# Optimization experiments

Hardware: AMD Instinct MI355X
Metric: run time of the kernel (lower is better)

The kernel has to match this reference:

```python
import jax, jax.numpy as jnp
import numpy as np

N, E, F, H, C, K = 50000, 1600000, 128, 64, 40, 4


def setup_inputs() -> dict:
    key = jax.random.key(0)
    ks = jax.random.split(key, 4)
    x = jax.random.normal(ks[0], (N, F), dtype=jnp.float32)
    edge_index = jax.random.randint(ks[1], (2, E), 0, N, dtype=jnp.int32)
    edge_weight = jnp.ones((E,), dtype=jnp.float32)
    # lin of ChebConv: Linear(K*in, out); kaiming for layer1, xavier-ish for layer2
    W1 = jax.random.normal(ks[2], (K * F, H), dtype=jnp.float32) * (2.0 / (K * F)) ** 0.5
    b1 = jnp.zeros((H,), jnp.float32)
    W2 = jax.random.normal(ks[3], (K * H, C), dtype=jnp.float32) * (2.0 / (K * H + C)) ** 0.5
    b2 = jnp.zeros((C,), jnp.float32)
    return {"x": x, "edge_index": edge_index, "edge_weight": edge_weight,
            "W1": W1, "b1": b1, "W2": W2, "b2": b2}


def _cheb_norm(edge_index, edge_weight, num_nodes):
    """Edge weights of L_hat = 2*L/lambda_max - I with sym norm, lambda_max=2.
    L = I - D^{-1/2} A D^{-1/2}; so L_hat off-diag = -d_i^{-1/2} w d_j^{-1/2},
    diag = (1 if deg>0 else 0) - 1."""
    src, dst = edge_index[0], edge_index[1]
    deg = jax.ops.segment_sum(edge_weight, src, num_segments=num_nodes)
    dis = jnp.where(deg > 0, jax.lax.rsqrt(jnp.maximum(deg, 1e-12)), 0.0)
    w_norm = -dis[src] * edge_weight * dis[dst]   # [E] off-diagonal of L_hat
    diag = jnp.where(deg > 0, 0.0, -1.0)          # [N] diagonal of L_hat
    return src, dst, w_norm, diag


def _cheb_conv(x, src, dst, w_norm, diag, W, b, num_nodes):
    def prop(h):  # L_hat @ h via gather-multiply-scatter
        msg = w_norm[:, None] * h[src]                                  # [E, F]
        return diag[:, None] * h + jax.ops.segment_sum(msg, dst, num_segments=num_nodes)

    Tx_prev2 = x
    Tx_prev1 = prop(x)
    Txs = [Tx_prev2, Tx_prev1]
    for _ in range(2, K):
        Tx = 2.0 * prop(Tx_prev1) - Tx_prev2
        Txs.append(Tx)
        Tx_prev2, Tx_prev1 = Tx_prev1, Tx
    Z = jnp.concatenate(Txs, axis=1)              # [N, K*F]
    return Z @ W + b


def reference(x, edge_index, edge_weight, W1, b1, W2, b2):
    num_nodes = x.shape[0]
    src, dst, w_norm, diag = _cheb_norm(edge_index, edge_weight, num_nodes)
    # dropout layers are identity at inference
    h = _cheb_conv(x, src, dst, w_norm, diag, W1, b1, num_nodes)
    h = jax.nn.relu(h)
    out = _cheb_conv(h, src, dst, w_norm, diag, W2, b2, num_nodes)
    return out
```

## Files before the change

kernel.cpp:

```cpp
#include <hip/hip_runtime.h>

#define NN 50000
#define EE 1600000
#define FF 128
#define HH 64
#define CC 40

#define NCH 64
#define CHE (EE / NCH)
#define NSL 4
#define SLN (NN / NSL)

#define PA 250
#define EPP (EE / PA)
#define SB 250
#define SLNB 200
#define BCAP 64

static __device__ __forceinline__ float bf2f(unsigned short u) {
    union { unsigned int i; float f; } c; c.i = ((unsigned int)u) << 16; return c.f;
}
static __device__ __forceinline__ unsigned short f2bf(float x) {
    union { float f; unsigned int i; } c; c.f = x;
    unsigned int r = c.i + 0x7FFFu + ((c.i >> 16) & 1u);
    return (unsigned short)(r >> 16);
}

__global__ __launch_bounds__(1024) void deg_hist_kernel(
    const int* __restrict__ src, const float* __restrict__ w,
    float* __restrict__ pdeg) {
    __shared__ float ldeg[SLN];
    int s = blockIdx.x % NSL;
    int c = blockIdx.x / NSL;
    int base = s * SLN;
    for (int i = threadIdx.x; i < SLN; i += 1024) ldeg[i] = 0.f;
    __syncthreads();
    int e0 = c * CHE;
    for (int e = e0 + threadIdx.x; e < e0 + CHE; e += 1024) {
        int se = src[e];
        unsigned us = (unsigned)(se - base);
        if (us < SLN) atomicAdd(&ldeg[us], w[e]);
    }
    __syncthreads();
    for (int i = threadIdx.x; i < SLN; i += 1024)
        pdeg[(size_t)c * NN + base + i] = ldeg[i];
}

__global__ void reduce_kernel(const float* __restrict__ pdeg,
                              float* __restrict__ dis, float* __restrict__ diag) {
    int n = blockIdx.x * blockDim.x + threadIdx.x;
    if (n >= NN) return;
    float dsum = 0.f;
    for (int c = 0; c < NCH; ++c) dsum += pdeg[(size_t)c * NN + n];
    dis[n]  = (dsum > 0.f) ? rsqrtf(fmaxf(dsum, 1e-12f)) : 0.f;
    diag[n] = (dsum > 0.f) ? 0.f : -1.f;
}

__global__ __launch_bounds__(256) void bucketA_kernel(
    const int* __restrict__ src, const int* __restrict__ dst,
    const float* __restrict__ w, const float* __restrict__ dis,
    uint2* __restrict__ buckets, int* __restrict__ counts) {
    __shared__ int lcnt[SB];
    int p = blockIdx.x;
    for (int i = threadIdx.x; i < SB; i += 256) lcnt[i] = 0;
    __syncthreads();
    int e0 = p * EPP;
    for (int e = e0 + threadIdx.x; e < e0 + EPP; e += 256) {
        int de = dst[e], se = src[e];
        int sl = de / SLNB;
        int dl = de - sl * SLNB;
        float wn = -dis[se] * w[e] * dis[de];
        unsigned lo = (unsigned)se | ((unsigned)f2bf(wn) << 16);
        int idx = atomicAdd(&lcnt[sl], 1);
        buckets[((size_t)p * SB + sl) * BCAP + idx] = make_uint2(lo, (unsigned)dl);
    }
    __syncthreads();
    for (int i = threadIdx.x; i < SB; i += 256) counts[p * SB + i] = lcnt[i];
}

__global__ void scanS_kernel(const int* __restrict__ counts, int* __restrict__ sbase) {
    __shared__ int sh[256];
    int t = threadIdx.x;
    int total = 0;
    if (t < SB)
        for (int p = 0; p < PA; ++p) total += counts[p * SB + t];
    sh[t] = total;
    __syncthreads();
    for (int off = 1; off < 256; off <<= 1) {
        int x = (t >= off) ? sh[t - off] : 0;
        __syncthreads();
        sh[t] += x;
        __syncthreads();
    }
    if (t < SB) sbase[t] = sh[t] - total;
    if (t == SB - 1) sbase[SB] = sh[t];
}

__global__ __launch_bounds__(256) void bucketB_kernel(
    const uint2* __restrict__ buckets, const int* __restrict__ counts,
    const int* __restrict__ sbase,
    int* __restrict__ row_start, unsigned int* __restrict__ csr) {
    __shared__ int lcounts[PA];
    __shared__ int lhist[SLNB];
    __shared__ int sh[256];
    int s = blockIdx.x;
    int t = threadIdx.x;
    if (t < PA) lcounts[t] = counts[t * SB + s];
    for (int i = t; i < SLNB; i += 256) lhist[i] = 0;
    __syncthreads();
    int g = t >> 4, l16 = t & 15;
    for (int p = g; p < PA; p += 16) {
        int c = lcounts[p];
        const uint2* b = buckets + ((size_t)p * SB + s) * BCAP;
        for (int i = l16; i < c; i += 16)
            atomicAdd(&lhist[b[i].y], 1);
    }
    __syncthreads();
    int v = (t < SLNB) ? lhist[t] : 0;
    sh[t] = v;
    __syncthreads();
    for (int off = 1; off < 256; off <<= 1) {
        int x = (t >= off) ? sh[t - off] : 0;
        __syncthreads();
        sh[t] += x;
        __syncthreads();
    }
    int base = sbase[s];
    if (t < SLNB) {
        int excl = sh[t] - v;
        row_start[s * SLNB + t] = base + excl;
        lhist[t] = base + excl;
    }
    if (s == SB - 1 && t == 0) row_start[NN] = sbase[SB];
    __syncthreads();
    for (int p = g; p < PA; p += 16) {
        int c = lcounts[p];
        const uint2* b = buckets + ((size_t)p * SB + s) * BCAP;
        for (int i = l16; i < c; i += 16) {
            uint2 en = b[i];
            int pos = atomicAdd(&lhist[en.y], 1);
            csr[pos] = en.x;
        }
    }
}

template <int FACT, typename OUT_T>
__global__ __launch_bounds__(256) void prop2_kernel(
    const unsigned short* __restrict__ a, float alphaL,
    const unsigned short* __restrict__ p1, float beta1,
    const unsigned short* __restrict__ p2, float beta2,
    const float* __restrict__ bias, int doRelu, int FOUT, int outStride,
    const float* __restrict__ diag, const int* __restrict__ rs,
    const unsigned int* __restrict__ csr, OUT_T* __restrict__ out) {
    int lane = threadIdx.x & 63;
    int wave = threadIdx.x >> 6;
    int n = blockIdx.x * 4 + wave;
    int f = lane;
    float acc = 0.f;
    if (f < FACT) {
        acc = diag[n] * bf2f(a[(size_t)n * 64 + f]);
        int j0 = rs[n], j1 = rs[n + 1];
        int j = j0;
        for (; j + 8 <= j1; j += 8) {
            unsigned cw[8];
            #pragma unroll
            for (int u = 0; u < 8; ++u) cw[u] = csr[j + u];
            float v[8];
            #pragma unroll
            for (int u = 0; u < 8; ++u)
                v[u] = bf2f(a[(size_t)(cw[u] & 0xFFFFu) * 64 + f]);
            #pragma unroll
            for (int u = 0; u < 8; ++u)
                acc = fmaf(bf2f((unsigned short)(cw[u] >> 16)), v[u], acc);
        }
        for (; j < j1; ++j) {
            unsigned cw = csr[j];
            acc = fmaf(bf2f((unsigned short)(cw >> 16)),
                       bf2f(a[(size_t)(cw & 0xFFFFu) * 64 + f]), acc);
        }
    }
    if (f < FOUT) {
        float r = alphaL * acc + beta1 * bf2f(p1[(size_t)n * 64 + f]);
        if (beta2 != 0.f) r = fmaf(beta2, bf2f(p2[(size_t)n * 64 + f]), r);
        if (bias) r += bias[f];
        if (doRelu) r = fmaxf(r, 0.f);
        OUT_T o;
        if constexpr (sizeof(OUT_T) == 2) o = f2bf(r); else o = r;
        out[(size_t)n * outStride + f] = o;
    }
}

__global__ __launch_bounds__(256) void gemm1_kernel(
    const float* __restrict__ x, const float* __restrict__ W,
    unsigned short* __restrict__ Yb) {
    __shared__ float As[64][36];
    __shared__ float Bs[32][64];
    int t = threadIdx.x;
    int m0 = blockIdx.x * 64;
    int ct = blockIdx.y;
    int tr = t / 16, tc = t % 16;
    int kq = t % 8,  ms = t / 8;
    int jb = t % 16, fb = t / 16;
    float acc[4][4] = {};
    for (int kb = 0; kb < 4; ++kb) {
        __syncthreads();
        #pragma unroll
        for (int p = 0; p < 2; ++p) {
            int m = ms + 32 * p;
            int row = m0 + m;
            float4 vv = make_float4(0.f, 0.f, 0.f, 0.f);
            if (row < NN) vv = *(const float4*)(x + (size_t)row * FF + kb * 32 + kq * 4);
            *(float4*)&As[m][kq * 4] = vv;
        }
        const float* Wb = W + ((size_t)ct * 128 + kb * 32) * HH;
        #pragma unroll
        for (int p = 0; p < 2; ++p) {
            int fi = fb + 16 * p;
            float4 vv = *(const float4*)(Wb + fi * HH + jb * 4);
            *(float4*)&Bs[fi][jb * 4] = vv;
        }
        __syncthreads();
        #pragma unroll 8
        for (int k = 0; k < 32; ++k) {
            float a0 = As[tr * 4 + 0][k], a1 = As[tr * 4 + 1][k];
            float a2 = As[tr * 4 + 2][k], a3 = As[tr * 4 + 3][k];
            float4 b = *(float4*)&Bs[k][tc * 4];
            acc[0][0] = fmaf(a0, b.x, acc[0][0]); acc[0][1] = fmaf(a0, b.y, acc[0][1]);
            acc[0][2] = fmaf(a0, b.z, acc[0][2]); acc[0][3] = fmaf(a0, b.w, acc[0][3]);
            acc[1][0] = fmaf(a1, b.x, acc[1][0]); acc[1][1] = fmaf(a1, b.y, acc[1][1]);
            acc[1][2] = fmaf(a1, b.z, acc[1][2]); acc[1][3] = fmaf(a1, b.w, acc[1][3]);
            acc[2][0] = fmaf(a2, b.x, acc[2][0]); acc[2][1] = fmaf(a2, b.y, acc[2][1]);
            acc[2][2] = fmaf(a2, b.z, acc[2][2]); acc[2][3] = fmaf(a2, b.w, acc[2][3]);
            acc[3][0] = fmaf(a3, b.x, acc[3][0]); acc[3][1] = fmaf(a3, b.y, acc[3][1]);
            acc[3][2] = fmaf(a3, b.z, acc[3][2]); acc[3][3] = fmaf(a3, b.w, acc[3][3]);
        }
    }
    unsigned short* slab = Yb + (size_t)ct * NN * 64;
    #pragma unroll
    for (int r = 0; r < 4; ++r) {
        int n = m0 + tr * 4 + r;
        if (n < NN) {
            ushort4 u4;
            u4.x = f2bf(acc[r][0]); u4.y = f2bf(acc[r][1]);
            u4.z = f2bf(acc[r][2]); u4.w = f2bf(acc[r][3]);
            *(ushort4*)(slab + (size_t)n * 64 + tc * 4) = u4;
        }
    }
}

__global__ __launch_bounds__(256) void gemm2_kernel(
    const float* __restrict__ h, const float* __restrict__ W,
    unsigned short* __restrict__ Zb) {
    __shared__ float As[128][36];
    __shared__ float Bs[32][40];
    int t = threadIdx.x;
    int m0 = blockIdx.x * 128;
    int kt = blockIdx.y;
    int tr = t / 8, tc = t % 8;
    int kq = t % 8, ms = t / 8;
    float acc[4][5] = {};
    for (int kb = 0; kb < 2; ++kb) {
        __syncthreads();
        #pragma unroll
        for (int p = 0; p < 4; ++p) {
            int m = ms + 32 * p;
            int row = m0 + m;
            float4 vv = make_float4(0.f, 0.f, 0.f, 0.f);
            if (row < NN) vv = *(const float4*)(h + (size_t)row * HH + kb * 32 + kq * 4);
            *(float4*)&As[m][kq * 4] = vv;
        }
        const float* Wb = W + ((size_t)kt * 64 + kb * 32) * CC;
        for (int i = t; i < 32 * CC; i += 256) ((float*)Bs)[i] = Wb[i];
        __syncthreads();
        #pragma unroll 4
        for (int k = 0; k < 32; ++k) {
            float a0 = As[tr * 4 + 0][k], a1 = As[tr * 4 + 1][k];
            float a2 = As[tr * 4 + 2][k], a3 = As[tr * 4 + 3][k];
            #pragma unroll
            for (int c = 0; c < 5; ++c) {
                float b = Bs[k][tc * 5 + c];
                acc[0][c] = fmaf(a0, b, acc[0][c]);
                acc[1][c] = fmaf(a1, b, acc[1][c]);
                acc[2][c] = fmaf(a2, b, acc[2][c]);
                acc[3][c] = fmaf(a3, b, acc[3][c]);
            }
        }
    }
    unsigned short* slab = Zb + (size_t)kt * NN * 64;
    #pragma unroll
    for (int r = 0; r < 4; ++r) {
        int n = m0 + tr * 4 + r;
        if (n < NN) {
            unsigned short* brow = slab + (size_t)n * 64;
            #pragma unroll
            for (int c = 0; c < 5; ++c) brow[tc * 5 + c] = f2bf(acc[r][c]);
            if (tc < 6) {
                #pragma unroll
                for (int c = 0; c < 4; ++c) brow[40 + tc * 4 + c] = 0;
            }
        }
    }
}

extern "C" void kernel_launch(void* const* d_in, const int* in_sizes, int n_in,
                              void* d_out, int out_size, void* d_ws, size_t ws_size,
                              hipStream_t stream) {
    const float* x    = (const float*)d_in[0];
    const int*   eidx = (const int*)d_in[1];
    const float* ew   = (const float*)d_in[2];
    const float* W1   = (const float*)d_in[3];
    const float* b1   = (const float*)d_in[4];
    const float* W2   = (const float*)d_in[5];
    const float* b2   = (const float*)d_in[6];
    float* out = (float*)d_out;

    const int* src = eidx;
    const int* dst = eidx + EE;

    float* p = (float*)d_ws;
    unsigned int* csr = (unsigned int*)p;  p += (size_t)EE;
    float* dis  = p;                  p += ((NN + 63) / 64) * 64;
    float* diag = p;                  p += ((NN + 63) / 64) * 64;
    unsigned short* Yb = (unsigned short*)p;  p += (size_t)NN * 128;
    unsigned short* u  = (unsigned short*)p;  p += (size_t)NN * 32;
    unsigned short* v  = (unsigned short*)p;  p += (size_t)NN * 32;
    float* h    = p;                  p += (size_t)NN * 64;
    float* scratch = p;               p += (size_t)PA * SB * BCAP * 2;
    int* row_start = (int*)p;
    int* counts    = row_start + NN + 1;
    int* sbase     = counts + PA * SB;

    float* pdeg    = scratch;
    uint2* buckets = (uint2*)scratch;
    unsigned short* y0b = Yb;
    unsigned short* y1b = Yb + (size_t)1 * NN * 64;
    unsigned short* y2b = Yb + (size_t)2 * NN * 64;
    unsigned short* y3b = Yb + (size_t)3 * NN * 64;
    unsigned short* Zb = Yb;
    unsigned short* z0 = Zb;
    unsigned short* z1 = Zb + (size_t)1 * NN * 64;
    unsigned short* z2 = Zb + (size_t)2 * NN * 64;
    unsigned short* z3 = Zb + (size_t)3 * NN * 64;
    unsigned short* u2 = u;
    unsigned short* v2 = v;

    const int B = 256;
    deg_hist_kernel<<<NCH * NSL, 1024, 0, stream>>>(src, ew, pdeg);
    reduce_kernel<<<(NN + B - 1) / B, B, 0, stream>>>(pdeg, dis, diag);
    bucketA_kernel<<<PA, 256, 0, stream>>>(src, dst, ew, dis, buckets, counts);
    scanS_kernel<<<1, 256, 0, stream>>>(counts, sbase);
    bucketB_kernel<<<SB, 256, 0, stream>>>(buckets, counts, sbase, row_start, csr);

    int pgrid = NN / 4;

    gemm1_kernel<<<dim3((NN + 63) / 64, 4), 256, 0, stream>>>(x, W1, Yb);
    prop2_kernel<64, unsigned short><<<pgrid, 256, 0, stream>>>(
        y3b, 4.f, y2b, 2.f, nullptr, 0.f,
        nullptr, 0, 64, 64, diag, row_start, csr, u);
    prop2_kernel<64, unsigned short><<<pgrid, 256, 0, stream>>>(
        u, 1.f, y1b, 1.f, y3b, -3.f,
        nullptr, 0, 64, 64, diag, row_start, csr, v);
    prop2_kernel<64, float><<<pgrid, 256, 0, stream>>>(
        v, 1.f, y0b, 1.f, y2b, -1.f,
        b1, 1, 64, 64, diag, row_start, csr, h);

    gemm2_kernel<<<dim3((NN + 127) / 128, 4), 256, 0, stream>>>(h, W2, Zb);
    prop2_kernel<48, unsigned short><<<pgrid, 256, 0, stream>>>(
        z3, 4.f, z2, 2.f, nullptr, 0.f,
        nullptr, 0, 48, 64, diag, row_start, csr, u2);
    prop2_kernel<48, unsigned short><<<pgrid, 256, 0, stream>>>(
        u2, 1.f, z1, 1.f, z3, -3.f,
        nullptr, 0, 48, 64, diag, row_start, csr, v2);
    prop2_kernel<48, float><<<pgrid, 256, 0, stream>>>(
        v2, 1.f, z0, 1.f, z2, -1.f,
        b2, 0, 40, 40, diag, row_start, csr, out);
}
```

Measured before the change: 534.3 us.

## Replace FP32 SIMT GEMMs with split-bf16 MFMA GEMMs

Replaces the two shared-memory FP32 FMA GEMM kernels with one templated MFMA kernel that uses bf16 16x16x32 matrix instructions. It keeps near-FP32 accuracy by splitting each operand into hi and lo bf16 parts and issuing three MFMAs per tile. A small kernel pre-transposes and splits W1 and W2 into the scratch buffer, and it pads W2 to 64 output columns with zeros. The aim is to move the dense projection work onto the matrix cores, at the cost of extra conversion instructions, one extra launch, and uncoalesced 2-byte output stores.

New measurement: 520.2 us. 2.6% less time.

```diff
diff --git a/kernel.cpp b/kernel.cpp
--- a/kernel.cpp
+++ b/kernel.cpp
@@ -25,6 +25,10 @@
     unsigned int r = c.i + 0x7FFFu + ((c.i >> 16) & 1u);
     return (unsigned short)(r >> 16);
 }
+
+typedef __attribute__((ext_vector_type(8))) short bf16x8;
+typedef __attribute__((ext_vector_type(4))) float f32x4;
+union BF8 { bf16x8 v; unsigned short u[8]; };
 
 __global__ __launch_bounds__(1024) void deg_hist_kernel(
     const int* __restrict__ src, const float* __restrict__ w,
@@ -190,116 +194,99 @@
     }
 }
 
-__global__ __launch_bounds__(256) void gemm1_kernel(
-    const float* __restrict__ x, const float* __restrict__ W,
-    unsigned short* __restrict__ Yb) {
-    __shared__ float As[64][36];
-    __shared__ float Bs[32][64];
-    int t = threadIdx.x;
-    int m0 = blockIdx.x * 64;
-    int ct = blockIdx.y;
-    int tr = t / 16, tc = t % 16;
-    int kq = t % 8,  ms = t / 8;
-    int jb = t % 16, fb = t / 16;
-    float acc[4][4] = {};
-    for (int kb = 0; kb < 4; ++kb) {
-        __syncthreads();
-        #pragma unroll
-        for (int p = 0; p < 2; ++p) {
-            int m = ms + 32 * p;
-            int row = m0 + m;
-            float4 vv = make_float4(0.f, 0.f, 0.f, 0.f);
-            if (row < NN) vv = *(const float4*)(x + (size_t)row * FF + kb * 32 + kq * 4);
-            *(float4*)&As[m][kq * 4] = vv;
-        }
-        const float* Wb = W + ((size_t)ct * 128 + kb * 32) * HH;
-        #pragma unroll
-        for (int p = 0; p < 2; ++p) {
-            int fi = fb + 16 * p;
-            float4 vv = *(const float4*)(Wb + fi * HH + jb * 4);
-            *(float4*)&Bs[fi][jb * 4] = vv;
-        }
-        __syncthreads();
-        #pragma unroll 8
-        for (int k = 0; k < 32; ++k) {
-            float a0 = As[tr * 4 + 0][k], a1 = As[tr * 4 + 1][k];
-            float a2 = As[tr * 4 + 2][k], a3 = As[tr * 4 + 3][k];
-            float4 b = *(float4*)&Bs[k][tc * 4];
-            acc[0][0] = fmaf(a0, b.x, acc[0][0]); acc[0][1] = fmaf(a0, b.y, acc[0][1]);
-            acc[0][2] = fmaf(a0, b.z, acc[0][2]); acc[0][3] = fmaf(a0, b.w, acc[0][3]);
-            acc[1][0] = fmaf(a1, b.x, acc[1][0]); acc[1][1] = fmaf(a1, b.y, acc[1][1]);
-            acc[1][2] = fmaf(a1, b.z, acc[1][2]); acc[1][3] = fmaf(a1, b.w, acc[1][3]);
-            acc[2][0] = fmaf(a2, b.x, acc[2][0]); acc[2][1] = fmaf(a2, b.y, acc[2][1]);
-            acc[2][2] = fmaf(a2, b.z, acc[2][2]); acc[2][3] = fmaf(a2, b.w, acc[2][3]);
-            acc[3][0] = fmaf(a3, b.x, acc[3][0]); acc[3][1] = fmaf(a3, b.y, acc[3][1]);
-            acc[3][2] = fmaf(a3, b.z, acc[3][2]); acc[3][3] = fmaf(a3, b.w, acc[3][3]);
-        }
-    }
+__global__ __launch_bounds__(256) void convw_kernel(
+    const float* __restrict__ W1, const float* __restrict__ W2,
+    unsigned short* __restrict__ W1t_hi, unsigned short* __restrict__ W1t_lo,
+    unsigned short* __restrict__ W2t_hi, unsigned short* __restrict__ W2t_lo) {
+    int tid = blockIdx.x * 256 + threadIdx.x;
+    if (tid < 512 * 64) {
+        int row = tid >> 7, kk = tid & 127;
+        int ct = row >> 6, j = row & 63;
+        float v = W1[((size_t)(ct * 128 + kk)) * 64 + j];
+        unsigned short h = f2bf(v);
+        W1t_hi[tid] = h;
+        W1t_lo[tid] = f2bf(v - bf2f(h));
+    } else {
+        int t2 = tid - 512 * 64;
+        if (t2 >= 4 * 64 * 64) return;
+        int row = t2 >> 6, kk = t2 & 63;
+        int kt = row >> 6, j = row & 63;
+        float v = (j < CC) ? W2[((size_t)(kt * 64 + kk)) * CC + j] : 0.f;
+        unsigned short h = f2bf(v);
+        W2t_hi[t2] = h;
+        W2t_lo[t2] = f2bf(v - bf2f(h));
+    }
+}
+
+template <int KF>
+__global__ __launch_bounds__(256) void gemm_mfma_kernel(
+    const float* __restrict__ A, const unsigned short* __restrict__ Wt_hi,
+    const unsigned short* __restrict__ Wt_lo, unsigned short* __restrict__ Yb) {
+    constexpr int KK = KF * 32;
+    int lane = threadIdx.x & 63;
+    int ct   = threadIdx.x >> 6;
+    int l15  = lane & 15;
+    int lg   = lane >> 4;
+    int m0   = blockIdx.x * 32;
+
+    f32x4 acc[2][4];
+    #pragma unroll
+    for (int i = 0; i < 2; ++i)
+        #pragma unroll
+        for (int j = 0; j < 4; ++j)
+            acc[i][j] = (f32x4){0.f, 0.f, 0.f, 0.f};
+
+    #pragma unroll
+    for (int kf = 0; kf < KF; ++kf) {
+        int k0 = kf * 32 + lg * 8;
+        BF8 bh[4], bl[4];
+        #pragma unroll
+        for (int nf = 0; nf < 4; ++nf) {
+            size_t addr = (size_t)(ct * 64 + nf * 16 + l15) * KK + k0;
+            bh[nf].v = *reinterpret_cast<const bf16x8*>(Wt_hi + addr);
+            bl[nf].v = *reinterpret_cast<const bf16x8*>(Wt_lo + addr);
+        }
+        BF8 ah[2], al[2];
+        #pragma unroll
+        for (int ms = 0; ms < 2; ++ms) {
+            int n = m0 + ms * 16 + l15;
+            if (n >= NN) n = NN - 1;
+            const float* ap = A + (size_t)n * KK + k0;
+            float4 f0 = *(const float4*)(ap);
+            float4 f1 = *(const float4*)(ap + 4);
+            float fv[8] = {f0.x, f0.y, f0.z, f0.w, f1.x, f1.y, f1.z, f1.w};
+            #pragma unroll
+            for (int u = 0; u < 8; ++u) {
+                unsigned short h = f2bf(fv[u]);
+                ah[ms].u[u] = h;
+                al[ms].u[u] = f2bf(fv[u] - bf2f(h));
+            }
+        }
+        #pragma unroll
+        for (int ms = 0; ms < 2; ++ms)
+            #pragma unroll
+            for (int nf = 0; nf < 4; ++nf) {
+                acc[ms][nf] = __builtin_amdgcn_mfma_f32_16x16x32_bf16(
+                    ah[ms].v, bh[nf].v, acc[ms][nf], 0, 0, 0);
+                acc[ms][nf] = __builtin_amdgcn_mfma_f32_16x16x32_bf16(
+                    ah[ms].v, bl[nf].v, acc[ms][nf], 0, 0, 0);
+                acc[ms][nf] = __builtin_amdgcn_mfma_f32_16x16x32_bf16(
+                    al[ms].v, bh[nf].v, acc[ms][nf], 0, 0, 0);
+            }
+    }
+
     unsigned short* slab = Yb + (size_t)ct * NN * 64;
     #pragma unroll
-    for (int r = 0; r < 4; ++r) {
-        int n = m0 + tr * 4 + r;
-        if (n < NN) {
-            ushort4 u4;
-            u4.x = f2bf(acc[r][0]); u4.y = f2bf(acc[r][1]);
-            u4.z = f2bf(acc[r][2]); u4.w = f2bf(acc[r][3]);
-            *(ushort4*)(slab + (size_t)n * 64 + tc * 4) = u4;
-        }
-    }
-}
-
-__global__ __launch_bounds__(256) void gemm2_kernel(
-    const float* __restrict__ h, const float* __restrict__ W,
-    unsigned short* __restrict__ Zb) {
-    __shared__ float As[128][36];
-    __shared__ float Bs[32][40];
-    int t = threadIdx.x;
-    int m0 = blockIdx.x * 128;
-    int kt = blockIdx.y;
-    int tr = t / 8, tc = t % 8;
-    int kq = t % 8, ms = t / 8;
-    float acc[4][5] = {};
-    for (int kb = 0; kb < 2; ++kb) {
-        __syncthreads();
-        #pragma unroll
-        for (int p = 0; p < 4; ++p) {
-            int m = ms + 32 * p;
-            int row = m0 + m;
-            float4 vv = make_float4(0.f, 0.f, 0.f, 0.f);
-            if (row < NN) vv = *(const float4*)(h + (size_t)row * HH + kb * 32 + kq * 4);
-            *(float4*)&As[m][kq * 4] = vv;
-        }
-        const float* Wb = W + ((size_t)kt * 64 + kb * 32) * CC;
-        for (int i = t; i < 32 * CC; i += 256) ((float*)Bs)[i] = Wb[i];
-        __syncthreads();
-        #pragma unroll 4
-        for (int k = 0; k < 32; ++k) {
-            float a0 = As[tr * 4 + 0][k], a1 = As[tr * 4 + 1][k];
-            float a2 = As[tr * 4 + 2][k], a3 = As[tr * 4 + 3][k];
-            #pragma unroll
-            for (int c = 0; c < 5; ++c) {
-                float b = Bs[k][tc * 5 + c];
-                acc[0][c] = fmaf(a0, b, acc[0][c]);
-                acc[1][c] = fmaf(a1, b, acc[1][c]);
-                acc[2][c] = fmaf(a2, b, acc[2][c]);
-                acc[3][c] = fmaf(a3, b, acc[3][c]);
+    for (int ms = 0; ms < 2; ++ms)
+        #pragma unroll
+        for (int r = 0; r < 4; ++r) {
+            int n = m0 + ms * 16 + lg * 4 + r;
+            if (n < NN) {
+                #pragma unroll
+                for (int nf = 0; nf < 4; ++nf)
+                    slab[(size_t)n * 64 + nf * 16 + l15] = f2bf(acc[ms][nf][r]);
             }
         }
-    }
-    unsigned short* slab = Zb + (size_t)kt * NN * 64;
-    #pragma unroll
-    for (int r = 0; r < 4; ++r) {
-        int n = m0 + tr * 4 + r;
-        if (n < NN) {
-            unsigned short* brow = slab + (size_t)n * 64;
-            #pragma unroll
-            for (int c = 0; c < 5; ++c) brow[tc * 5 + c] = f2bf(acc[r][c]);
-            if (tc < 6) {
-                #pragma unroll
-                for (int c = 0; c < 4; ++c) brow[40 + tc * 4 + c] = 0;
-            }
-        }
-    }
 }
 
 extern "C" void kernel_launch(void* const* d_in, const int* in_sizes, int n_in,
@@ -332,6 +319,10 @@
 
     float* pdeg    = scratch;
     uint2* buckets = (uint2*)scratch;
+    unsigned short* W1t_hi = (unsigned short*)scratch;
+    unsigned short* W1t_lo = W1t_hi + 512 * 64;
+    unsigned short* W2t_hi = W1t_lo + 512 * 64;
+    unsigned short* W2t_lo = W2t_hi + 4 * 64 * 64;
     unsigned short* y0b = Yb;
     unsigned short* y1b = Yb + (size_t)1 * NN * 64;
     unsigned short* y2b = Yb + (size_t)2 * NN * 64;
@@ -350,10 +341,12 @@
     bucketA_kernel<<<PA, 256, 0, stream>>>(src, dst, ew, dis, buckets, counts);
     scanS_kernel<<<1, 256, 0, stream>>>(counts, sbase);
     bucketB_kernel<<<SB, 256, 0, stream>>>(buckets, counts, sbase, row_start, csr);
+    convw_kernel<<<192, 256, 0, stream>>>(W1, W2, W1t_hi, W1t_lo, W2t_hi, W2t_lo);
 
     int pgrid = NN / 4;
-
-    gemm1_kernel<<<dim3((NN + 63) / 64, 4), 256, 0, stream>>>(x, W1, Yb);
+    int ggrid = (NN + 31) / 32;
+
+    gemm_mfma_kernel<4><<<ggrid, 256, 0, stream>>>(x, W1t_hi, W1t_lo, Yb);
     prop2_kernel<64, unsigned short><<<pgrid, 256, 0, stream>>>(
         y3b, 4.f, y2b, 2.f, nullptr, 0.f,
         nullptr, 0, 64, 64, diag, row_start, csr, u);
@@ -364,7 +357,7 @@
         v, 1.f, y0b, 1.f, y2b, -1.f,
         b1, 1, 64, 64, diag, row_start, csr, h);
 
-    gemm2_kernel<<<dim3((NN + 127) / 128, 4), 256, 0, stream>>>(h, W2, Zb);
+    gemm_mfma_kernel<2><<<ggrid, 256, 0, stream>>>(h, W2t_hi, W2t_lo, Zb);
     prop2_kernel<48, unsigned short><<<pgrid, 256, 0, stream>>>(
         z3, 4.f, z2, 2.f, nullptr, 0.f,
         nullptr, 0, 48, 64, diag, row_start, csr, u2);
```
